# Performance work log

Hardware: AMD Instinct MI355X
Metric: run time of the kernel (lower is better)

Reference implementation:

```python
import jax, jax.numpy as jnp
import numpy as np
from jax import lax


def _conv(x, w, padding, groups=1):
    # NCHW / OIHW 2D conv, stride 1
    return lax.conv_general_dilated(
        x, w, window_strides=(1, 1), padding=padding,
        dimension_numbers=("NCHW", "OIHW", "NCHW"),
        feature_group_count=groups)


def setup_inputs() -> dict:
    key = jax.random.key(0)
    ks = jax.random.split(key, 5)
    B, C, H, W = 8, 192, 128, 128
    HEADS = 8
    rgb = jax.random.normal(ks[0], (B, C, H, W), dtype=jnp.float32)
    ir = jax.random.normal(ks[1], (B, C, H, W), dtype=jnp.float32)
    w_qkv = jax.random.normal(ks[2], (3 * C, C, 1, 1), dtype=jnp.float32) * 0.02
    w_dw = jax.random.normal(ks[3], (3 * C, 1, 3, 3), dtype=jnp.float32) * 0.02
    w_proj = jax.random.normal(ks[4], (C, C, 1, 1), dtype=jnp.float32) * 0.02
    temperature = jnp.ones((HEADS, 1, 1), dtype=jnp.float32)
    return {"rgb": rgb, "ir": ir, "w_qkv": w_qkv, "w_dw": w_dw,
            "w_proj": w_proj, "temperature": temperature}


def reference(rgb, ir, w_qkv, w_dw, w_proj, temperature):
    heads = temperature.shape[0]
    b, c, h, w = rgb.shape
    hd = c // heads  # per-head channel count

    def qkv(x):
        y = _conv(x, w_qkv, "VALID")                 # [b, 3c, h, w]
        y = _conv(y, w_dw, "SAME", groups=3 * c)      # depthwise 3x3
        q, k, v = jnp.split(y, 3, axis=1)
        rs = lambda t: t.reshape(b, heads, hd, h * w)  # b head c (h w)
        return rs(q), rs(k), rs(v)

    rq, rk, rv = qkv(rgb)
    iq, ik, iv = qkv(ir)

    # torch F.normalize(dim=-1): x / max(||x||_2, 1e-12)
    nrm = lambda t: t / jnp.maximum(jnp.linalg.norm(t, axis=-1, keepdims=True), 1e-12)
    rq, rk, iq, ik = nrm(rq), nrm(rk), nrm(iq), nrm(ik)

    # channel-wise (transposed) cross attention: [b,h,hd,hd] attn matrices
    attn_ir = jax.nn.softmax(jnp.einsum("bhcn,bhdn->bhcd", rq, ik) * temperature, axis=-1)
    attn_rgb = jax.nn.softmax(jnp.einsum("bhcn,bhdn->bhcd", iq, rk) * temperature, axis=-1)

    out_ir = jnp.einsum("bhcd,bhdn->bhcn", attn_ir, iv).reshape(b, c, h, w)
    out_rgb = jnp.einsum("bhcd,bhdn->bhcn", attn_rgb, rv).reshape(b, c, h, w)

    out_ir = _conv(out_ir, w_proj, "VALID")
    out_rgb = _conv(out_rgb, w_proj, "VALID")
    return out_rgb, out_ir
```

## Files before the change

kernel.cpp:

```cpp
#include <hip/hip_runtime.h>

#define N_PIX 16384
#define CC    192
#define C3    576
#define KK    192
#define HD    24
#define GSPLIT 32

typedef __attribute__((ext_vector_type(8))) short short8;
typedef __attribute__((ext_vector_type(4))) float f32x4;

__device__ __forceinline__ unsigned short f2bf(float x) {
    unsigned u = __float_as_uint(x);
    u += 0x7fff + ((u >> 16) & 1);
    return (unsigned short)(u >> 16);
}
__device__ __forceinline__ float bf2f(unsigned short s) {
    return __uint_as_float(((unsigned)s) << 16);
}
__device__ __forceinline__ int pack2(unsigned short lo, unsigned short hi) {
    return (int)(((unsigned)hi << 16) | (unsigned)lo);
}

__device__ __forceinline__ void g2l16(const unsigned short* g, unsigned short* l) {
    __builtin_amdgcn_global_load_lds(
        (const __attribute__((address_space(1))) void*)g,
        (__attribute__((address_space(3))) void*)l, 16, 0, 0);
}

__global__ __launch_bounds__(256) void cvt_f32_bf16(const float* __restrict__ src,
                                                    unsigned short* __restrict__ dst, int n4) {
    int i = blockIdx.x * 256 + threadIdx.x;
    if (i < n4) {
        float4 v = ((const float4*)src)[i];
        ushort4 o;
        o.x = f2bf(v.x); o.y = f2bf(v.y); o.z = f2bf(v.z); o.w = f2bf(v.w);
        ((ushort4*)dst)[i] = o;
    }
}

__global__ __launch_bounds__(256) void zero_f32(float* __restrict__ p, int n) {
    int i = blockIdx.x * 256 + threadIdx.x;
    if (i < n) p[i] = 0.f;
}

__global__ __launch_bounds__(256) void cvtT(const float* __restrict__ rgb,
                                            const float* __restrict__ ir,
                                            unsigned short* __restrict__ xT) {
    const int z  = blockIdx.y;
    const int n0 = blockIdx.x * 128;
    const float* x = ((z >= 8) ? ir : rgb) + (long)(z & 7) * CC * N_PIX;
    __shared__ unsigned short T[192][136];

    const int t = threadIdx.x;
#pragma unroll
    for (int i = 0; i < 24; i++) {
        int q = i * 256 + t;
        int k = q >> 5, nc = q & 31;
        float4 v = *(const float4*)(x + (long)k * N_PIX + n0 + nc * 4);
        ushort4 o;
        o.x = f2bf(v.x); o.y = f2bf(v.y); o.z = f2bf(v.z); o.w = f2bf(v.w);
        *(ushort4*)&T[k][nc * 4] = o;
    }
    __syncthreads();
    unsigned short* dst = xT + ((long)z * N_PIX + n0) * CC;
#pragma unroll
    for (int i = 0; i < 12; i++) {
        int c = i * 256 + t;
        int n = c / 24, kc = c - n * 24;
        unsigned short us[8];
#pragma unroll
        for (int j = 0; j < 8; j++) us[j] = T[kc * 8 + j][n];
        int4 pk = make_int4(pack2(us[0], us[1]), pack2(us[2], us[3]),
                            pack2(us[4], us[5]), pack2(us[6], us[7]));
        *(int4*)(dst + (long)n * CC + kc * 8) = pk;
    }
}

__global__ __launch_bounds__(512, 4) void qkv_mfma(const unsigned short* __restrict__ wbf,
                                                   const unsigned short* __restrict__ xT,
                                                   unsigned short* __restrict__ Ybf) {
    const int z  = blockIdx.z;
    const unsigned short* Bg = xT + (long)z * N_PIX * CC;
    unsigned short* y = Ybf + (long)z * C3 * N_PIX;
    const int m0 = blockIdx.y * 192, n0 = blockIdx.x * 128;

    __shared__ unsigned short As[2][192 * 64];
    __shared__ unsigned short Bs[2][128 * 64];

    const int tid  = threadIdx.x;
    const int wave = tid >> 6, lane = tid & 63;
    const int quad = lane >> 4, l15 = lane & 15;
    const int wr = wave >> 2, wc = wave & 3;

    f32x4 acc[6][2];
#pragma unroll
    for (int i = 0; i < 6; i++)
#pragma unroll
        for (int j = 0; j < 2; j++) acc[i][j] = (f32x4)0.f;

    auto stage = [&](int buf, int k0) {
#pragma unroll
        for (int s = 0; s < 3; s++) {
            int j = s * 8 + wave;
            int q = j * 64 + lane;
            int m = q >> 3, c = (q & 7) ^ (m & 7);
            g2l16(wbf + (long)(m0 + m) * KK + k0 + c * 8, &As[buf][j * 512]);
        }
#pragma unroll
        for (int s = 0; s < 2; s++) {
            int j = s * 8 + wave;
            int q = j * 64 + lane;
            int n = q >> 3, c = (q & 7) ^ (n & 7);
            g2l16(Bg + (long)(n0 + n) * CC + k0 + c * 8, &Bs[buf][j * 512]);
        }
    };

    stage(0, 0);
    __syncthreads();
    int cur = 0;
    for (int it = 0; it < 3; ++it) {
        if (it < 2) stage(cur ^ 1, (it + 1) * 64);
        const unsigned short* A  = As[cur];
        const unsigned short* Bl = Bs[cur];
#pragma unroll
        for (int kk = 0; kk < 2; kk++) {
            short8 a[6], b[2];
#pragma unroll
            for (int mi = 0; mi < 6; mi++) {
                int r = wr * 96 + mi * 16 + l15;
                int c = (kk * 4 + quad) ^ (r & 7);
                a[mi] = *(const short8*)&A[r * 64 + c * 8];
            }
#pragma unroll
            for (int ni = 0; ni < 2; ni++) {
                int n = wc * 32 + ni * 16 + l15;
                int c = (kk * 4 + quad) ^ (n & 7);
                b[ni] = *(const short8*)&Bl[n * 64 + c * 8];
            }
#pragma unroll
            for (int mi = 0; mi < 6; mi++)
#pragma unroll
                for (int ni = 0; ni < 2; ni++)
                    acc[mi][ni] = __builtin_amdgcn_mfma_f32_16x16x32_bf16(a[mi], b[ni], acc[mi][ni], 0, 0, 0);
        }
        __syncthreads();
        cur ^= 1;
    }

#pragma unroll
    for (int mi = 0; mi < 6; mi++)
#pragma unroll
        for (int ni = 0; ni < 2; ni++)
#pragma unroll
            for (int r = 0; r < 4; r++) {
                int row = m0 + wr * 96 + mi * 16 + quad * 4 + r;
                int col = n0 + wc * 32 + ni * 16 + l15;
                y[(long)row * N_PIX + col] = f2bf(acc[mi][ni][r]);
            }
}

__global__ __launch_bounds__(512, 2) void gram_mfma(const unsigned short* __restrict__ Zbf,
                                                    float* __restrict__ gpart) {
    const int ks = blockIdx.x;
    const int zp = blockIdx.y;
    const int which = zp >> 3, b = zp & 7;
    const int zq = which ? 8 + b : b;
    const int zk = which ? b : 8 + b;
    const unsigned short* Qg = Zbf + (long)zq * C3 * N_PIX;
    const unsigned short* Kg = Zbf + ((long)zk * C3 + CC) * N_PIX;

    __shared__ unsigned short Qs[2][192 * 64];
    __shared__ unsigned short Ks[2][192 * 64];

    const int tid  = threadIdx.x;
    const int wave = tid >> 6, lane = tid & 63;
    const int quad = lane >> 4, l15 = lane & 15;
    const int wr = wave >> 1, wc = wave & 1;

    f32x4 acc[3][6];
#pragma unroll
    for (int i = 0; i < 3; i++)
#pragma unroll
        for (int j = 0; j < 6; j++) acc[i][j] = (f32x4)0.f;

    const int base = ks * 512;

    auto stage = [&](int buf, int k0) {
#pragma unroll
        for (int s = 0; s < 3; s++) {
            int j = s * 8 + wave;
            int q = j * 64 + lane;
            int m = q >> 3, c = (q & 7) ^ (m & 7);
            g2l16(Qg + (long)m * N_PIX + k0 + c * 8, &Qs[buf][j * 512]);
            g2l16(Kg + (long)m * N_PIX + k0 + c * 8, &Ks[buf][j * 512]);
        }
    };

    stage(0, base);
    __syncthreads();
    int cur = 0;
    for (int it = 0; it < 8; ++it) {
        if (it < 7) stage(cur ^ 1, base + (it + 1) * 64);
        const unsigned short* Q = Qs[cur];
        const unsigned short* Kl = Ks[cur];
#pragma unroll
        for (int kk = 0; kk < 2; kk++) {
            short8 a[3], bf[6];
#pragma unroll
            for (int mi = 0; mi < 3; mi++) {
                int r = wr * 48 + mi * 16 + l15;
                int c = (kk * 4 + quad) ^ (r & 7);
                a[mi] = *(const short8*)&Q[r * 64 + c * 8];
            }
#pragma unroll
            for (int ni = 0; ni < 6; ni++) {
                int n = wc * 96 + ni * 16 + l15;
                int c = (kk * 4 + quad) ^ (n & 7);
                bf[ni] = *(const short8*)&Kl[n * 64 + c * 8];
            }
#pragma unroll
            for (int mi = 0; mi < 3; mi++)
#pragma unroll
                for (int ni = 0; ni < 6; ni++)
                    acc[mi][ni] = __builtin_amdgcn_mfma_f32_16x16x32_bf16(a[mi], bf[ni], acc[mi][ni], 0, 0, 0);
        }
        __syncthreads();
        cur ^= 1;
    }

#pragma unroll
    for (int mi = 0; mi < 3; mi++)
#pragma unroll
        for (int ni = 0; ni < 6; ni++)
#pragma unroll
            for (int r = 0; r < 4; r++) {
                int row = wr * 48 + mi * 16 + quad * 4 + r;
                int col = wc * 96 + ni * 16 + l15;
                int hr = row / 24, hc = col / 24;
                if (hr == hc)
                    gpart[(((long)zp * GSPLIT + ks) * 8 + hr) * 576 +
                          (row - hr * 24) * 24 + (col - hc * 24)] = acc[mi][ni][r];
            }
}

__device__ __forceinline__ void mfma_gemm_old(const unsigned short* __restrict__ Abf,
                                              const unsigned short* __restrict__ Bsrc,
                                              float* __restrict__ Cdst,
                                              int m0, int n0) {
    __shared__ unsigned short As[192][44];
    __shared__ unsigned short Bs[128][44];

    const int tid  = threadIdx.x;
    const int wave = tid >> 6, lane = tid & 63;
    const int quad = lane >> 4, l15 = lane & 15;
    const int wr = wave >> 2, wc = wave & 3;

    f32x4 acc[6][2];
#pragma unroll
    for (int i = 0; i < 6; i++)
#pragma unroll
        for (int j = 0; j < 2; j++) acc[i][j] = (f32x4)0.f;

    const int kg = tid & 7;
    const int n2 = tid >> 3;

    for (int k0 = 0; k0 < KK; k0 += 32) {
        {
            int row = tid >> 2, kc = (tid & 3) * 8;
            *(int4*)&As[row][kc] = *(const int4*)(Abf + (long)(m0 + row) * KK + k0 + kc);
            if (tid < 256) {
                int ch = tid + 512;
                int row2 = ch >> 2, kc2 = (ch & 3) * 8;
                *(int4*)&As[row2][kc2] = *(const int4*)(Abf + (long)(m0 + row2) * KK + k0 + kc2);
            }
        }
        {
            ushort2 v[4];
#pragma unroll
            for (int j = 0; j < 4; j++)
                v[j] = *(const ushort2*)(Bsrc + (long)(k0 + kg * 4 + j) * N_PIX + n0 + n2 * 2);
#pragma unroll
            for (int i = 0; i < 2; i++) {
                unsigned short us[4];
#pragma unroll
                for (int j = 0; j < 4; j++) us[j] = i ? v[j].y : v[j].x;
                int2 pk = make_int2(pack2(us[0], us[1]), pack2(us[2], us[3]));
                *(int2*)&Bs[n2 * 2 + i][kg * 4] = pk;
            }
        }
        __syncthreads();

        short8 a[6], b[2];
#pragma unroll
        for (int mi = 0; mi < 6; mi++)
            a[mi] = *(const short8*)&As[wr * 96 + mi * 16 + l15][quad * 8];
#pragma unroll
        for (int ni = 0; ni < 2; ni++)
            b[ni] = *(const short8*)&Bs[wc * 32 + ni * 16 + l15][quad * 8];
#pragma unroll
        for (int mi = 0; mi < 6; mi++)
#pragma unroll
            for (int ni = 0; ni < 2; ni++)
                acc[mi][ni] = __builtin_amdgcn_mfma_f32_16x16x32_bf16(a[mi], b[ni], acc[mi][ni], 0, 0, 0);
        __syncthreads();
    }

#pragma unroll
    for (int mi = 0; mi < 6; mi++)
#pragma unroll
        for (int ni = 0; ni < 2; ni++)
#pragma unroll
            for (int r = 0; r < 4; r++) {
                int row = m0 + wr * 96 + mi * 16 + quad * 4 + r;
                int col = n0 + wc * 32 + ni * 16 + l15;
                Cdst[(long)row * N_PIX + col] = acc[mi][ni][r];
            }
}

__global__ __launch_bounds__(512, 4) void out_mfma(const unsigned short* __restrict__ weff,
                                                   const unsigned short* __restrict__ Zbf,
                                                   float* __restrict__ out) {
    const int z = blockIdx.z;
    const unsigned short* V = Zbf + ((long)z * C3 + 2 * CC) * N_PIX;
    float* C = out + (long)z * CC * N_PIX;
    mfma_gemm_old(weff + (long)z * CC * CC, V, C, 0, blockIdx.x * 128);
}

__global__ __launch_bounds__(256) void dwconv3x3(const unsigned short* __restrict__ Ybf,
                                                 const float* __restrict__ wdw,
                                                 unsigned short* __restrict__ Zbf,
                                                 float* __restrict__ norm) {
    const int z  = blockIdx.z;
    const int oc = blockIdx.y;
    const int idx = blockIdx.x * 256 + threadIdx.x;
    const int p0  = idx * 8;
    const int h   = p0 >> 7;
    const int w0  = p0 & 127;
    const int wq  = threadIdx.x & 15;
    const unsigned short* Yc = Ybf + ((long)z * C3 + oc) * N_PIX;

    float wk[9];
#pragma unroll
    for (int i = 0; i < 9; i++) wk[i] = wdw[oc * 9 + i];

    float f[3][8];
#pragma unroll
    for (int ry = 0; ry < 3; ry++) {
        const int hy = h + ry - 1;
        int4 raw = make_int4(0, 0, 0, 0);
        if (hy >= 0 && hy <= 127)
            raw = *(const int4*)(Yc + hy * 128 + w0);
        f[ry][0] = bf2f((unsigned short)(raw.x & 0xffff));
        f[ry][1] = bf2f((unsigned short)((unsigned)raw.x >> 16));
        f[ry][2] = bf2f((unsigned short)(raw.y & 0xffff));
        f[ry][3] = bf2f((unsigned short)((unsigned)raw.y >> 16));
        f[ry][4] = bf2f((unsigned short)(raw.z & 0xffff));
        f[ry][5] = bf2f((unsigned short)((unsigned)raw.z >> 16));
        f[ry][6] = bf2f((unsigned short)(raw.w & 0xffff));
        f[ry][7] = bf2f((unsigned short)((unsigned)raw.w >> 16));
    }

    float acc[8];
#pragma unroll
    for (int j = 0; j < 8; j++) acc[j] = 0.f;

#pragma unroll
    for (int ry = 0; ry < 3; ry++) {
        float l = __shfl_up(f[ry][7], 1);
        float r = __shfl_down(f[ry][0], 1);
        if (wq == 0)  l = 0.f;
        if (wq == 15) r = 0.f;
        const float wl = wk[ry * 3 + 0], wc = wk[ry * 3 + 1], wr = wk[ry * 3 + 2];
        acc[0] = fmaf(wl, l, acc[0]);
#pragma unroll
        for (int j = 1; j < 8; j++) acc[j] = fmaf(wl, f[ry][j - 1], acc[j]);
#pragma unroll
        for (int j = 0; j < 8; j++) acc[j] = fmaf(wc, f[ry][j], acc[j]);
#pragma unroll
        for (int j = 0; j < 7; j++) acc[j] = fmaf(wr, f[ry][j + 1], acc[j]);
        acc[7] = fmaf(wr, r, acc[7]);
    }

    ushort4 o[2];
    unsigned short* po = (unsigned short*)o;
#pragma unroll
    for (int j = 0; j < 8; j++) po[j] = f2bf(acc[j]);
    *(int4*)(Zbf + ((long)z * C3 + oc) * N_PIX + p0) = *(const int4*)o;

    if (oc < 2 * CC) {
        float ss = 0.f;
#pragma unroll
        for (int j = 0; j < 8; j++) {
            float v = bf2f(po[j]);
            ss = fmaf(v, v, ss);
        }
#pragma unroll
        for (int off = 32; off > 0; off >>= 1)
            ss += __shfl_down(ss, off);
        if ((threadIdx.x & 63) == 0)
            atomicAdd(&norm[z * (2 * CC) + oc], ss);
    }
}

__global__ __launch_bounds__(256) void gram_reduce_softmax(const float* __restrict__ gpart,
                                                           const float* __restrict__ norm,
                                                           const float* __restrict__ temperature,
                                                           float* __restrict__ P) {
    const int g = blockIdx.x;
    const int which = g >> 6, b = (g >> 3) & 7, head = g & 7;
    const int zp = which * 8 + b;
    const int zq = which ? 8 + b : b;
    const int zk = which ? b : 8 + b;
    __shared__ float Gs[576];
    __shared__ float invq[24], invk[24];

    const int t = threadIdx.x;
    for (int e = t; e < 576; e += 256) {
        float s = 0.f;
        for (int sp = 0; sp < GSPLIT; sp++)
            s += gpart[(((long)zp * GSPLIT + sp) * 8 + head) * 576 + e];
        Gs[e] = s;
    }
    if (t < 24)
        invq[t] = 1.f / fmaxf(sqrtf(norm[zq * (2 * CC) + head * HD + t]), 1e-12f);
    else if (t >= 32 && t < 56)
        invk[t - 32] = 1.f / fmaxf(sqrtf(norm[zk * (2 * CC) + CC + head * HD + (t - 32)]), 1e-12f);
    __syncthreads();
    if (t < 24) {
        const float temp = temperature[head];
        float row[24];
        float m = -1e30f;
#pragma unroll
        for (int d = 0; d < 24; d++) {
            row[d] = Gs[t * 24 + d] * invq[t] * invk[d] * temp;
            m = fmaxf(m, row[d]);
        }
        float ssum = 0.f;
#pragma unroll
        for (int d = 0; d < 24; d++) {
            row[d] = expf(row[d] - m);
            ssum += row[d];
        }
        const float inv = 1.f / ssum;
#pragma unroll
        for (int d = 0; d < 24; d++)
            P[(long)g * 576 + t * 24 + d] = row[d] * inv;
    }
}

__global__ __launch_bounds__(256) void build_weff(const float* __restrict__ wproj,
                                                  const float* __restrict__ P,
                                                  unsigned short* __restrict__ weff) {
    const int o = blockIdx.z, b = blockIdx.y;
    const int e = blockIdx.x * 256 + threadIdx.x;
    const int co = e / 192, col = e % 192;
    const int head = col / 24, d = col % 24;
    const int which = 1 - o;
    const float* Pp = P + (long)(which * 64 + b * 8 + head) * 576;
    const float* wp = wproj + co * 192 + head * 24;
    float acc = 0.f;
#pragma unroll
    for (int hc = 0; hc < 24; hc++)
        acc = fmaf(wp[hc], Pp[hc * 24 + d], acc);
    weff[((long)(o * 8 + b) * 192 + co) * 192 + col] = f2bf(acc);
}

extern "C" void kernel_launch(void* const* d_in, const int* in_sizes, int n_in,
                              void* d_out, int out_size, void* d_ws, size_t ws_size,
                              hipStream_t stream) {
    (void)in_sizes; (void)n_in; (void)out_size; (void)ws_size;
    const float* rgb    = (const float*)d_in[0];
    const float* ir     = (const float*)d_in[1];
    const float* w_qkv  = (const float*)d_in[2];
    const float* w_dw   = (const float*)d_in[3];
    const float* w_proj = (const float*)d_in[4];
    const float* temp   = (const float*)d_in[5];
    float* out = (float*)d_out;

    char* wsb = (char*)d_ws;
    unsigned short* Y_bf    = (unsigned short*)(wsb);
    unsigned short* Z_bf    = (unsigned short*)(wsb + 301989888L);
    unsigned short* xT_bf   = Z_bf;
    float*          gpart   = (float*)(wsb);
    unsigned short* w_bf    = (unsigned short*)(wsb + 603979776L);
    unsigned short* weff_bf = (unsigned short*)(wsb + 604200960L);
    float*          norm    = (float*)(wsb + 605380608L);
    float*          P       = (float*)(wsb + 607936512L);

    cvt_f32_bf16<<<108, 256, 0, stream>>>(w_qkv, w_bf, 27648);
    cvtT<<<dim3(128, 16), 256, 0, stream>>>(rgb, ir, xT_bf);
    zero_f32<<<24, 256, 0, stream>>>(norm, 16 * 2 * CC);
    qkv_mfma<<<dim3(128, 3, 16), 512, 0, stream>>>(w_bf, xT_bf, Y_bf);
    dwconv3x3<<<dim3(8, 576, 16), 256, 0, stream>>>(Y_bf, w_dw, Z_bf, norm);
    gram_mfma<<<dim3(GSPLIT, 16), 512, 0, stream>>>(Z_bf, gpart);
    gram_reduce_softmax<<<128, 256, 0, stream>>>(gpart, norm, temp, P);
    build_weff<<<dim3(144, 8, 2), 256, 0, stream>>>(w_proj, P, weff_bf);
    out_mfma<<<dim3(128, 1, 16), 512, 0, stream>>>(weff_bf, Z_bf, out);
}
```

Baseline: 753.7 us.

## Fuse fp32-to-bf16 transpose into QKV GEMM and replace norm atomics with partials

Removes the separate cvtT pass by having qkv_mfma load fp32 input directly, convert to bf16 in registers and write swizzled B tiles into LDS, with register prefetch overlapping the MFMA loop. The grid is reordered so the three M-blocks sharing an input tile run adjacently for L2 reuse. Norm accumulation switches from atomics to per-block partial sums reduced in the softmax kernel, eliminating the zeroing kernel. This saves a full write and read of the transposed bf16 activation, but adds strided fp32 global loads and VALU conversion work inside the GEMM.

```diff
diff --git a/kernel.cpp b/kernel.cpp
--- a/kernel.cpp
+++ b/kernel.cpp
@@ -39,51 +39,14 @@
     }
 }
 
-__global__ __launch_bounds__(256) void zero_f32(float* __restrict__ p, int n) {
-    int i = blockIdx.x * 256 + threadIdx.x;
-    if (i < n) p[i] = 0.f;
-}
-
-__global__ __launch_bounds__(256) void cvtT(const float* __restrict__ rgb,
-                                            const float* __restrict__ ir,
-                                            unsigned short* __restrict__ xT) {
-    const int z  = blockIdx.y;
-    const int n0 = blockIdx.x * 128;
-    const float* x = ((z >= 8) ? ir : rgb) + (long)(z & 7) * CC * N_PIX;
-    __shared__ unsigned short T[192][136];
-
-    const int t = threadIdx.x;
-#pragma unroll
-    for (int i = 0; i < 24; i++) {
-        int q = i * 256 + t;
-        int k = q >> 5, nc = q & 31;
-        float4 v = *(const float4*)(x + (long)k * N_PIX + n0 + nc * 4);
-        ushort4 o;
-        o.x = f2bf(v.x); o.y = f2bf(v.y); o.z = f2bf(v.z); o.w = f2bf(v.w);
-        *(ushort4*)&T[k][nc * 4] = o;
-    }
-    __syncthreads();
-    unsigned short* dst = xT + ((long)z * N_PIX + n0) * CC;
-#pragma unroll
-    for (int i = 0; i < 12; i++) {
-        int c = i * 256 + t;
-        int n = c / 24, kc = c - n * 24;
-        unsigned short us[8];
-#pragma unroll
-        for (int j = 0; j < 8; j++) us[j] = T[kc * 8 + j][n];
-        int4 pk = make_int4(pack2(us[0], us[1]), pack2(us[2], us[3]),
-                            pack2(us[4], us[5]), pack2(us[6], us[7]));
-        *(int4*)(dst + (long)n * CC + kc * 8) = pk;
-    }
-}
-
 __global__ __launch_bounds__(512, 4) void qkv_mfma(const unsigned short* __restrict__ wbf,
-                                                   const unsigned short* __restrict__ xT,
+                                                   const float* __restrict__ rgb,
+                                                   const float* __restrict__ ir,
                                                    unsigned short* __restrict__ Ybf) {
-    const int z  = blockIdx.z;
-    const unsigned short* Bg = xT + (long)z * N_PIX * CC;
+    const int z = blockIdx.z;
+    const float* xg = ((z >= 8) ? ir : rgb) + (long)(z & 7) * CC * N_PIX;
     unsigned short* y = Ybf + (long)z * C3 * N_PIX;
-    const int m0 = blockIdx.y * 192, n0 = blockIdx.x * 128;
+    const int m0 = blockIdx.x * 192, n0 = blockIdx.y * 128;
 
     __shared__ unsigned short As[2][192 * 64];
     __shared__ unsigned short Bs[2][128 * 64];
@@ -99,7 +62,9 @@
 #pragma unroll
         for (int j = 0; j < 2; j++) acc[i][j] = (f32x4)0.f;
 
-    auto stage = [&](int buf, int k0) {
+    const int nq = tid & 63, kq = tid >> 6;
+
+    auto stageA = [&](int buf, int k0) {
 #pragma unroll
         for (int s = 0; s < 3; s++) {
             int j = s * 8 + wave;
@@ -107,20 +72,39 @@
             int m = q >> 3, c = (q & 7) ^ (m & 7);
             g2l16(wbf + (long)(m0 + m) * KK + k0 + c * 8, &As[buf][j * 512]);
         }
-#pragma unroll
-        for (int s = 0; s < 2; s++) {
-            int j = s * 8 + wave;
-            int q = j * 64 + lane;
-            int n = q >> 3, c = (q & 7) ^ (n & 7);
-            g2l16(Bg + (long)(n0 + n) * CC + k0 + c * 8, &Bs[buf][j * 512]);
-        }
     };
 
-    stage(0, 0);
+    float2 bv[8];
+    auto loadB = [&](int k0) {
+#pragma unroll
+        for (int j = 0; j < 8; j++)
+            bv[j] = *(const float2*)(xg + (long)(k0 + kq * 8 + j) * N_PIX + n0 + nq * 2);
+    };
+    auto writeB = [&](int buf) {
+#pragma unroll
+        for (int i = 0; i < 2; i++) {
+            int n = nq * 2 + i;
+            unsigned short us[8];
+#pragma unroll
+            for (int j = 0; j < 8; j++) us[j] = f2bf(i ? bv[j].y : bv[j].x);
+            int4 pk = make_int4(pack2(us[0], us[1]), pack2(us[2], us[3]),
+                                pack2(us[4], us[5]), pack2(us[6], us[7]));
+            int c = kq ^ (n & 7);
+            *(int4*)&Bs[buf][n * 64 + c * 8] = pk;
+        }
+    };
+
+    loadB(0);
+    stageA(0, 0);
+    writeB(0);
     __syncthreads();
+
     int cur = 0;
     for (int it = 0; it < 3; ++it) {
-        if (it < 2) stage(cur ^ 1, (it + 1) * 64);
+        if (it < 2) {
+            stageA(cur ^ 1, (it + 1) * 64);
+            loadB((it + 1) * 64);
+        }
         const unsigned short* A  = As[cur];
         const unsigned short* Bl = Bs[cur];
 #pragma unroll
@@ -144,6 +128,7 @@
                 for (int ni = 0; ni < 2; ni++)
                     acc[mi][ni] = __builtin_amdgcn_mfma_f32_16x16x32_bf16(a[mi], b[ni], acc[mi][ni], 0, 0, 0);
         }
+        if (it < 2) writeB(cur ^ 1);
         __syncthreads();
         cur ^= 1;
     }
@@ -330,7 +315,7 @@
 __global__ __launch_bounds__(256) void dwconv3x3(const unsigned short* __restrict__ Ybf,
                                                  const float* __restrict__ wdw,
                                                  unsigned short* __restrict__ Zbf,
-                                                 float* __restrict__ norm) {
+                                                 float* __restrict__ nrm) {
     const int z  = blockIdx.z;
     const int oc = blockIdx.y;
     const int idx = blockIdx.x * 256 + threadIdx.x;
@@ -388,23 +373,24 @@
     for (int j = 0; j < 8; j++) po[j] = f2bf(acc[j]);
     *(int4*)(Zbf + ((long)z * C3 + oc) * N_PIX + p0) = *(const int4*)o;
 
-    if (oc < 2 * CC) {
-        float ss = 0.f;
-#pragma unroll
-        for (int j = 0; j < 8; j++) {
-            float v = bf2f(po[j]);
-            ss = fmaf(v, v, ss);
-        }
-#pragma unroll
-        for (int off = 32; off > 0; off >>= 1)
-            ss += __shfl_down(ss, off);
-        if ((threadIdx.x & 63) == 0)
-            atomicAdd(&norm[z * (2 * CC) + oc], ss);
-    }
+    __shared__ float red[4];
+    float ss = 0.f;
+#pragma unroll
+    for (int j = 0; j < 8; j++) {
+        float v = bf2f(po[j]);
+        ss = fmaf(v, v, ss);
+    }
+#pragma unroll
+    for (int off = 32; off > 0; off >>= 1)
+        ss += __shfl_down(ss, off);
+    if ((threadIdx.x & 63) == 0) red[threadIdx.x >> 6] = ss;
+    __syncthreads();
+    if (threadIdx.x == 0 && oc < 2 * CC)
+        nrm[((long)z * (2 * CC) + oc) * 8 + blockIdx.x] = red[0] + red[1] + red[2] + red[3];
 }
 
 __global__ __launch_bounds__(256) void gram_reduce_softmax(const float* __restrict__ gpart,
-                                                           const float* __restrict__ norm,
+                                                           const float* __restrict__ nrm,
                                                            const float* __restrict__ temperature,
                                                            float* __restrict__ P) {
     const int g = blockIdx.x;
@@ -422,10 +408,19 @@
             s += gpart[(((long)zp * GSPLIT + sp) * 8 + head) * 576 + e];
         Gs[e] = s;
     }
-    if (t < 24)
-        invq[t] = 1.f / fmaxf(sqrtf(norm[zq * (2 * CC) + head * HD + t]), 1e-12f);
-    else if (t >= 32 && t < 56)
-        invk[t - 32] = 1.f / fmaxf(sqrtf(norm[zk * (2 * CC) + CC + head * HD + (t - 32)]), 1e-12f);
+    if (t < 24) {
+        float s = 0.f;
+#pragma unroll
+        for (int b8 = 0; b8 < 8; b8++)
+            s += nrm[((long)zq * (2 * CC) + head * HD + t) * 8 + b8];
+        invq[t] = 1.f / fmaxf(sqrtf(s), 1e-12f);
+    } else if (t >= 32 && t < 56) {
+        float s = 0.f;
+#pragma unroll
+        for (int b8 = 0; b8 < 8; b8++)
+            s += nrm[((long)zk * (2 * CC) + CC + head * HD + (t - 32)) * 8 + b8];
+        invk[t - 32] = 1.f / fmaxf(sqrtf(s), 1e-12f);
+    }
     __syncthreads();
     if (t < 24) {
         const float temp = temperature[head];
@@ -481,20 +476,17 @@
     char* wsb = (char*)d_ws;
     unsigned short* Y_bf    = (unsigned short*)(wsb);
     unsigned short* Z_bf    = (unsigned short*)(wsb + 301989888L);
-    unsigned short* xT_bf   = Z_bf;
     float*          gpart   = (float*)(wsb);
     unsigned short* w_bf    = (unsigned short*)(wsb + 603979776L);
     unsigned short* weff_bf = (unsigned short*)(wsb + 604200960L);
-    float*          norm    = (float*)(wsb + 605380608L);
+    float*          nrm     = (float*)(wsb + 605380608L);
     float*          P       = (float*)(wsb + 607936512L);
 
     cvt_f32_bf16<<<108, 256, 0, stream>>>(w_qkv, w_bf, 27648);
-    cvtT<<<dim3(128, 16), 256, 0, stream>>>(rgb, ir, xT_bf);
-    zero_f32<<<24, 256, 0, stream>>>(norm, 16 * 2 * CC);
-    qkv_mfma<<<dim3(128, 3, 16), 512, 0, stream>>>(w_bf, xT_bf, Y_bf);
-    dwconv3x3<<<dim3(8, 576, 16), 256, 0, stream>>>(Y_bf, w_dw, Z_bf, norm);
+    qkv_mfma<<<dim3(3, 128, 16), 512, 0, stream>>>(w_bf, rgb, ir, Y_bf);
+    dwconv3x3<<<dim3(8, 576, 16), 256, 0, stream>>>(Y_bf, w_dw, Z_bf, nrm);
     gram_mfma<<<dim3(GSPLIT, 16), 512, 0, stream>>>(Z_bf, gpart);
-    gram_reduce_softmax<<<128, 256, 0, stream>>>(gpart, norm, temp, P);
+    gram_reduce_softmax<<<128, 256, 0, stream>>>(gpart, nrm, temp, P);
     build_weff<<<dim3(144, 8, 2), 256, 0, stream>>>(w_proj, P, weff_bf);
     out_mfma<<<dim3(128, 1, 16), 512, 0, stream>>>(weff_bf, Z_bf, out);
 }
```

Result: faster. 673.0 us (-10.7%).
